# Kernel tuning notes

Measured on AMD Instinct MI355X. Metric: run time of the kernel, lower is better.

The kernel has to match this reference:

```python
import jax, jax.numpy as jnp
import numpy as np

K = 16
EPS = 1e-5
SLOPE = 0.2


def knn_idx(k, xyz_k, xyz_q):
    # xyz_k: (B,Nk,3), xyz_q: (B,Nq,3) -> (B,Nq,k) indices of k nearest in xyz_k
    d = (jnp.sum(xyz_q * xyz_q, -1, keepdims=True)
         - 2.0 * jnp.einsum('bqc,bkc->bqk', xyz_q, xyz_k)
         + jnp.sum(xyz_k * xyz_k, -1)[:, None, :])
    _, idx = jax.lax.top_k(-d, k)
    return idx


def graph_feature(coor_q, x_q, coor_k, x_k):
    # coor_*: (B,N*,3); x_q: (B,C,Nq); x_k: (B,C,Nk) -> (B,2C,Nq,K)
    idx = knn_idx(K, coor_k, coor_q)                      # (B,Nq,K)
    nbr = jax.vmap(lambda xk, i: xk[:, i])(x_k, idx)       # (B,C,Nq,K)
    xq = x_q[:, :, :, None]                                # (B,C,Nq,1)
    xq = jnp.broadcast_to(xq, nbr.shape)
    return jnp.concatenate([nbr - xq, xq], axis=1)


def group_norm(x, gamma, beta, groups=4):
    B, C, N, Kk = x.shape
    xg = x.reshape(B, groups, C // groups, N, Kk)
    mu = jnp.mean(xg, axis=(2, 3, 4), keepdims=True)
    var = jnp.var(xg, axis=(2, 3, 4), keepdims=True)
    xn = ((xg - mu) / jnp.sqrt(var + EPS)).reshape(B, C, N, Kk)
    return xn * gamma[None, :, None, None] + beta[None, :, None, None]


def cgl(f, W, gamma, beta):
    # 1x1 Conv2d (no bias) + GroupNorm(4) + LeakyReLU(0.2)
    y = jnp.einsum('oc,bcnk->bonk', W, f)
    return jax.nn.leaky_relu(group_norm(y, gamma, beta), SLOPE)


def fps(xyz, m):
    # furthest point sampling. xyz: (B,N,3) -> (B,m) int32
    B, N, _ = xyz.shape
    first = jnp.zeros((B,), jnp.int32)

    def body(carry, _):
        dist, last = carry
        lp = jnp.take_along_axis(xyz, last[:, None, None].astype(jnp.int32), axis=1)  # (B,1,3)
        d = jnp.sum((xyz - lp) ** 2, -1)
        dist = jnp.minimum(dist, d)
        nxt = jnp.argmax(dist, -1).astype(jnp.int32)
        return (dist, nxt), nxt

    init = (jnp.full((B, N), 1e10, jnp.float32), first)
    _, rest = jax.lax.scan(body, init, None, length=m - 1)  # (m-1,B)
    return jnp.concatenate([first[None, :], rest], axis=0).T  # (B,m)


def fps_downsample(coor, x, m):
    # coor: (B,N,3), x: (B,C,N) -> new_coor (B,3,m), new_x (B,C,m)
    idx = fps(coor, m)                                        # (B,m)
    new_coor = jnp.take_along_axis(coor, idx[:, :, None], axis=1).transpose(0, 2, 1)
    new_x = jnp.take_along_axis(x, idx[:, None, :], axis=2)
    return new_coor, new_x


def setup_inputs() -> dict:
    key = jax.random.key(0)
    ks = jax.random.split(key, 16)
    d = {
        'x': jax.random.normal(ks[0], (8, 4096, 3), jnp.float32),
        'num0': 2048, 'num1': 512, 'num2': 128,
        'w_in': jax.random.normal(ks[1], (8, 3), jnp.float32) * 0.3,
        'b_in': jnp.zeros((8,), jnp.float32),
    }
    layer_dims = {'1': (32, 16), '2': (64, 64), '4': (128, 128),
                  '5': (128, 256), '6': (256, 256), '7': (256, 512)}
    for i, (name, (o, c)) in enumerate(layer_dims.items()):
        d[f'w{name}'] = jax.random.normal(ks[2 + i], (o, c), jnp.float32) * (1.0 / np.sqrt(c))
        d[f'g{name}'] = jnp.ones((o,), jnp.float32)
        d[f'be{name}'] = jnp.zeros((o,), jnp.float32)
    return d


def reference(x, num0, num1, num2, w_in, b_in,
              w1, g1, be1, w2, g2, be2, w4, g4, be4,
              w5, g5, be5, w6, g6, be6, w7, g7, be7):
    xyz = x.transpose(0, 2, 1)                                # (B,3,N)
    coor = x                                                  # (B,N,3)
    f = jnp.einsum('oc,bcn->bon', w_in, xyz) + b_in[None, :, None]  # (B,8,N)

    f = cgl(graph_feature(coor, f, coor, f), w1, g1, be1)     # (B,32,N,K)
    f = jnp.max(f, axis=-1)                                   # (B,32,N)

    sp1, f_q = fps_downsample(coor, f, num0)                  # (B,3,n0),(B,32,n0)
    coor_d = sp1.transpose(0, 2, 1)                           # (B,n0,3)
    f = cgl(graph_feature(coor_d, f_q, coor, f), w2, g2, be2)
    stage1_feature = jnp.max(f, axis=-1)                      # (B,64,n0)
    coor = coor_d

    sp2, f_q = fps_downsample(coor, stage1_feature, num1)
    coor_d = sp2.transpose(0, 2, 1)
    f = cgl(graph_feature(coor_d, f_q, coor, stage1_feature), w4, g4, be4)
    f = jnp.max(f, axis=-1)                                   # (B,128,n1)
    f = cgl(graph_feature(coor_d, f, coor_d, f), w5, g5, be5)
    stage2_feature = jnp.max(f, axis=-1)                      # (B,128,n1)
    coor = coor_d

    sp3, f_q = fps_downsample(coor, stage2_feature, num2)
    coor_d = sp3.transpose(0, 2, 1)
    f = cgl(graph_feature(coor_d, f_q, coor, stage2_feature), w6, g6, be6)
    f = jnp.max(f, axis=-1)                                   # (B,256,n2)
    f = cgl(graph_feature(coor_d, f, coor_d, f), w7, g7, be7)
    stage3_feature = jnp.max(f, axis=-1)                      # (B,256,n2)

    out_coor = sp3.transpose(0, 2, 1)                         # (B,n2,3)
    out_f = stage3_feature.transpose(0, 2, 1)                 # (B,n2,256)
    return out_coor, out_f
```

## Files before the change

### kernel.cpp

```cpp
#include <hip/hip_runtime.h>
#include <hip/hip_bf16.h>
#include <math.h>

#define DEVI __device__ __forceinline__
typedef unsigned long long ull;
typedef float f32x2 __attribute__((ext_vector_type(2)));

DEVI f32x2 pk_sub(f32x2 a, f32x2 b){
  f32x2 r;
  asm("v_pk_add_f32 %0, %1, %2 neg_lo:[0,1] neg_hi:[0,1]" : "=v"(r) : "v"(a), "v"(b));
  return r;
}
DEVI f32x2 pk_mul(f32x2 a, f32x2 b){
  f32x2 r; asm("v_pk_mul_f32 %0, %1, %2" : "=v"(r) : "v"(a), "v"(b)); return r;
}
DEVI f32x2 pk_add(f32x2 a, f32x2 b){
  f32x2 r; asm("v_pk_add_f32 %0, %1, %2" : "=v"(r) : "v"(a), "v"(b)); return r;
}

template<int CTRL>
DEVI float dppmaxf(float x){
  float o = __int_as_float(__builtin_amdgcn_update_dpp(__float_as_int(x),__float_as_int(x),CTRL,0xF,0xF,false));
  return fmaxf(x,o);
}
template<int CTRL>
DEVI unsigned dppminu(unsigned x){
  unsigned o = (unsigned)__builtin_amdgcn_update_dpp((int)x,(int)x,CTRL,0xF,0xF,false);
  return (x < o) ? x : o;
}

template<int P>
DEVI void fps_stage(f32x2 (&px)[P/2], f32x2 (&py)[P/2], f32x2 (&pz)[P/2],
                    int m, float sx, float sy, float sz,
                    const float* cpx, const float* cpy, const float* cpz,
                    ull* mK,
                    int* ssel, float* snx, float* sny, float* snz, int tid)
{
  const int wv = tid>>6, lane = tid&63;
  float dist[P];
  #pragma unroll
  for (int p=0;p<P;p++) dist[p]=1e10f;
  if (tid==0){ ssel[0]=0; if (snx){ snx[0]=sx; sny[0]=sy; snz[0]=sz; } }
  #pragma unroll 1
  for (int it=1; it<m; it++){
    f32x2 vsx, vsy, vsz;
    vsx.x=sx; vsx.y=sx; vsy.x=sy; vsy.y=sy; vsz.x=sz; vsz.y=sz;
    float bv = -1.f;
    #pragma unroll
    for (int i=0;i<P/2;i++){
      f32x2 dx = pk_sub(px[i], vsx);
      f32x2 dy = pk_sub(py[i], vsy);
      f32x2 dz = pk_sub(pz[i], vsz);
      f32x2 s  = pk_add(pk_add(pk_mul(dx,dx), pk_mul(dy,dy)), pk_mul(dz,dz));
      float d0 = fminf(dist[2*i],   s.x);
      float d1 = fminf(dist[2*i+1], s.y);
      dist[2*i] = d0; dist[2*i+1] = d1;
      bv = fmaxf(bv, d0);
      bv = fmaxf(bv, d1);
    }
    int bidx = 0;
    #pragma unroll
    for (int p=P-1;p>=0;p--) if (dist[p]==bv) bidx = tid+(p<<8);
    float w = bv;
    w = dppmaxf<0x111>(w);
    w = dppmaxf<0x112>(w);
    w = dppmaxf<0x114>(w);
    w = dppmaxf<0x118>(w);
    w = dppmaxf<0x142>(w);
    w = dppmaxf<0x143>(w);
    float bvw = __uint_as_float((unsigned)__builtin_amdgcn_readlane(__float_as_int(w),63));
    unsigned cand = (bv == bvw) ? (unsigned)bidx : 0xFFFFFFFFu;
    cand = dppminu<0x111>(cand);
    cand = dppminu<0x112>(cand);
    cand = dppminu<0x114>(cand);
    cand = dppminu<0x118>(cand);
    cand = dppminu<0x142>(cand);
    cand = dppminu<0x143>(cand);
    const unsigned itu = (unsigned)it;
    ull* slot = mK + ((it&1)<<2);
    if (lane==63){
      unsigned lo = ((~cand & 0xFFFu)<<12) | itu;
      *(volatile ull*)(slot + wv) = ((ull)__float_as_uint(bvw)<<32) | (ull)lo;
    }
    ull k0,k1,k2,k3;
    for (;;){
      asm volatile("" ::: "memory");
      k0=slot[0]; k1=slot[1]; k2=slot[2]; k3=slot[3];
      unsigned chk = (((unsigned)k0 ^ itu) | ((unsigned)k1 ^ itu) |
                      ((unsigned)k2 ^ itu) | ((unsigned)k3 ^ itu)) & 0xFFFu;
      if (chk == 0u) break;
    }
    ull ka = (k1>k0)?k1:k0;
    ull kb = (k3>k2)?k3:k2;
    ull kw = (kb>ka)?kb:ka;
    int gi = (int)((~((unsigned)(kw & 0xffffffffull) >> 12)) & 0xFFFu);
    sx = cpx[gi]; sy = cpy[gi]; sz = cpz[gi];
    if (tid==0){
      ssel[it]=gi;
      if (snx){ snx[it]=sx; sny[it]=sy; snz[it]=sz; }
    }
  }
}

template<int CTRL>
DEVI void dppmin_fj(float& d, int& j){
  float od = __int_as_float(__builtin_amdgcn_update_dpp(__float_as_int(d),__float_as_int(d),CTRL,0xF,0xF,false));
  int   oj = __builtin_amdgcn_update_dpp(j,j,CTRL,0xF,0xF,false);
  bool tk = (od < d) || (od == d && oj < j);
  d = tk?od:d; j = tk?oj:j;
}

DEVI float dist_qk(const float* __restrict__ ckb, int j,
                   float qx, float qy, float qz, float sqq){
  float kx=ckb[3*j], ky=ckb[3*j+1], kz=ckb[3*j+2];
  float sk  = __fadd_rn(__fadd_rn(__fmul_rn(kx,kx),__fmul_rn(ky,ky)),
                        __fmul_rn(kz,kz));
  float dot = __fadd_rn(__fadd_rn(__fmul_rn(qx,kx),__fmul_rn(qy,ky)),
                        __fmul_rn(qz,kz));
  return __fadd_rn(__fsub_rn(sqq, __fmul_rn(2.0f,dot)), sk);
}

template<int NPL>
DEVI void knn_wave(const float* __restrict__ cq, int Nq,
                   const float* __restrict__ ck, int Nk,
                   int* __restrict__ idx_out, int b, int q, int lane)
{
  size_t r3 = ((size_t)b*Nq+q)*3;
  float qx=cq[r3], qy=cq[r3+1], qz=cq[r3+2];
  float sqq = __fadd_rn(__fadd_rn(__fmul_rn(qx,qx),__fmul_rn(qy,qy)),
                        __fmul_rn(qz,qz));
  constexpr int GS = (NPL < 8) ? NPL : 8;
  constexpr int NG = NPL / GS;
  float gv[NG]; int gj[NG];
  const float* ckb = ck + (size_t)b*Nk*3;
  ull exmask = 0;
  int dirtyg = -1;
  int myout = 0;
  #pragma unroll 1
  for (int r=0; r<16; r++){
    #pragma unroll
    for (int g=0; g<NG; g++){
      if (dirtyg < 0 || dirtyg == g){
        float nv=__int_as_float(0x7f800000); int nj=0x7fffffff;
        #pragma unroll
        for (int e=0; e<GS; e++){
          const int i = g*GS+e;
          int j = lane + (i<<6);
          float d = dist_qk(ckb, j, qx,qy,qz, sqq);
          bool rem = ((exmask >> i) & 1ull) == 0ull;
          if (rem && d < nv){ nv=d; nj=j; }
        }
        gv[g]=nv; gj[g]=nj;
      }
    }
    float lv = gv[0]; int lj = gj[0];
    #pragma unroll
    for (int g=1; g<NG; g++)
      if (gv[g]<lv || (gv[g]==lv && gj[g]<lj)){ lv=gv[g]; lj=gj[g]; }
    float rd = lv; int rj = lj;
    dppmin_fj<0x111>(rd,rj);
    dppmin_fj<0x112>(rd,rj);
    dppmin_fj<0x114>(rd,rj);
    dppmin_fj<0x118>(rd,rj);
    dppmin_fj<0x142>(rd,rj);
    dppmin_fj<0x143>(rd,rj);
    int wj = __builtin_amdgcn_readlane(rj,63);
    if (lane == r) myout = wj;
    if ((wj & 63) == lane) exmask |= (1ull << (wj>>6));
    dirtyg = (wj>>6)/GS;
  }
  if (lane<16) idx_out[((size_t)b*Nq+q)*16 + lane] = myout;
}

__global__ __launch_bounds__(256) void k_fps_knn1(
    const float* __restrict__ coords0,
    int* __restrict__ idx1, int* __restrict__ idx2, int* __restrict__ idx3,
    float* __restrict__ c1, float* __restrict__ c2, float* __restrict__ c3,
    float* __restrict__ out, int* __restrict__ knn1,
    const float* __restrict__ w_in, const float* __restrict__ b_in,
    const float* __restrict__ wl1, const float* __restrict__ wq1,
    float* __restrict__ yk, float* __restrict__ yq)
{
  __shared__ float s1x[4096], s1y[4096], s1z[4096];
  __shared__ float s2x[2048], s2y[2048], s2z[2048];
  __shared__ float s3x[512],  s3y[512],  s3z[512];
  __shared__ float s4x[128],  s4y[128],  s4z[128];
  __shared__ int   ssel[2048];
  __shared__ alignas(32) ull mK[8];
  if (blockIdx.x >= 8 + 8192){
    const int g = blockIdx.x - 8200;
    const int b = g >> 6, bx = g & 63;
    const int tid = threadIdx.x;
    float* sf = s1x;
    const float* xb = coords0 + (size_t)b*4096*3;
    const int row0 = bx*64;
    for (int i=tid; i<64*8; i+=256){
      int r = i >> 3, c = i & 7;
      int row = row0 + r;
      float cx=xb[row*3], cy=xb[row*3+1], cz=xb[row*3+2];
      float s = __fadd_rn(__fadd_rn(__fmul_rn(cx,w_in[c*3+0]),
                                    __fmul_rn(cy,w_in[c*3+1])),
                          __fmul_rn(cz,w_in[c*3+2]));
      sf[r*9 + c] = __fadd_rn(s, b_in[c]);
    }
    __syncthreads();
    const int o = tid & 31, rg = tid >> 5;
    float ak[8], aq[8];
    #pragma unroll
    for (int m=0;m<8;m++){ ak[m]=0.f; aq[m]=0.f; }
    const float* lp = wl1 + o;
    const float* qp = wq1 + o;
    const float* sfr = sf + rg*8*9;
    #pragma unroll
    for (int c=0;c<8;c++){
      float wl = lp[c*32];
      float wq = qp[c*32];
      #pragma unroll
      for (int m=0;m<8;m++){
        float xv = sfr[m*9 + c];
        ak[m] = fmaf(xv, wl, ak[m]);
        aq[m] = fmaf(xv, wq, aq[m]);
      }
    }
    size_t obase = ((size_t)b*4096 + row0 + rg*8)*32 + o;
    #pragma unroll
    for (int m=0;m<8;m++){
      yk[obase + (size_t)m*32] = ak[m];
      yq[obase + (size_t)m*32] = aq[m];
    }
    return;
  }
  if (blockIdx.x >= 8){
    int flat = blockIdx.x - 8;
    int b = flat >> 10, qb = flat & 1023;
    int q = qb*4 + (threadIdx.x>>6);
    knn_wave<64>(coords0, 4096, coords0, 4096, knn1, b, q, threadIdx.x&63);
    return;
  }
  const int b = blockIdx.x, tid = threadIdx.x;
  __builtin_amdgcn_s_setprio(3);
  const float* cb = coords0 + (size_t)b*4096*3;
  if (tid<8) mK[tid] = ~0ull;
  {
    f32x2 px[8], py[8], pz[8];
    #pragma unroll
    for (int i=0;i<8;i++){
      int j0 = tid + ((2*i)<<8), j1 = tid + ((2*i+1)<<8);
      float X0=cb[3*j0], Y0=cb[3*j0+1], Z0=cb[3*j0+2];
      float X1=cb[3*j1], Y1=cb[3*j1+1], Z1=cb[3*j1+2];
      px[i].x=X0; px[i].y=X1; py[i].x=Y0; py[i].y=Y1; pz[i].x=Z0; pz[i].y=Z1;
      s1x[j0]=X0; s1y[j0]=Y0; s1z[j0]=Z0;
      s1x[j1]=X1; s1y[j1]=Y1; s1z[j1]=Z1;
    }
    float sx=cb[0], sy=cb[1], sz=cb[2];
    __syncthreads();
    fps_stage<16>(px,py,pz, 2048, sx,sy,sz, s1x,s1y,s1z,
                  mK, ssel, s2x,s2y,s2z, tid);
  }
  __syncthreads();
  {
    float* c1b = c1 + (size_t)b*2048*3;
    for (int i=tid;i<2048;i+=256){
      idx1[b*2048+i]=ssel[i];
      c1b[3*i]=s2x[i]; c1b[3*i+1]=s2y[i]; c1b[3*i+2]=s2z[i];
    }
  }
  {
    f32x2 px[4], py[4], pz[4];
    #pragma unroll
    for (int i=0;i<4;i++){
      int j0 = tid + ((2*i)<<8), j1 = tid + ((2*i+1)<<8);
      px[i].x=s2x[j0]; px[i].y=s2x[j1];
      py[i].x=s2y[j0]; py[i].y=s2y[j1];
      pz[i].x=s2z[j0]; pz[i].y=s2z[j1];
    }
    float sx=s2x[0], sy=s2y[0], sz=s2z[0];
    __syncthreads();
    fps_stage<8>(px,py,pz, 512, sx,sy,sz, s2x,s2y,s2z,
                 mK, ssel, s3x,s3y,s3z, tid);
  }
  __syncthreads();
  {
    float* c2b = c2 + (size_t)b*512*3;
    for (int i=tid;i<512;i+=256){
      idx2[b*512+i]=ssel[i];
      c2b[3*i]=s3x[i]; c2b[3*i+1]=s3y[i]; c2b[3*i+2]=s3z[i];
    }
  }
  {
    f32x2 px[1], py[1], pz[1];
    {
      int j0 = tid, j1 = tid + 256;
      px[0].x=s3x[j0]; px[0].y=s3x[j1];
      py[0].x=s3y[j0]; py[0].y=s3y[j1];
      pz[0].x=s3z[j0]; pz[0].y=s3z[j1];
    }
    float sx=s3x[0], sy=s3y[0], sz=s3z[0];
    __syncthreads();
    fps_stage<2>(px,py,pz, 128, sx,sy,sz, s3x,s3y,s3z,
                 mK, ssel, s4x,s4y,s4z, tid);
  }
  __syncthreads();
  {
    float* c3b = c3 + (size_t)b*128*3;
    float* ob  = out + (size_t)b*128*3;
    for (int i=tid;i<128;i+=256){
      idx3[b*128+i]=ssel[i];
      float X=s4x[i],Y=s4y[i],Z=s4z[i];
      c3b[3*i]=X; c3b[3*i+1]=Y; c3b[3*i+2]=Z;
      ob[3*i]=X; ob[3*i+1]=Y; ob[3*i+2]=Z;
    }
  }
}

struct WtParams {
  const float* W[6];
  float* wl[6];
  float* wq[6];
  int O[6], C[6], OC[6];
};
__global__ void k_wt_all(WtParams p, float* __restrict__ stats){
  int s = blockIdx.y;
  int t = blockIdx.x*blockDim.x + threadIdx.x;
  if (s==0 && t<384) stats[t] = 0.f;
  int OC = p.OC[s];
  if (t >= OC) return;
  int C = p.C[s], O = p.O[s];
  int o = t / C, c = t - o*C;
  const float* W = p.W[s];
  float wlv = W[o*2*C + c];
  float wrv = W[o*2*C + C + c];
  p.wl[s][c*O+o] = wlv;
  p.wq[s][c*O+o] = wrv - wlv;
}

#define GEMM_M 8
template<int NPL>
__global__ __launch_bounds__(256,3) void k_knn_gemm(
    const float* __restrict__ cq, int Nq,
    const float* __restrict__ ck, int Nk, int* __restrict__ knnidx,
    const float* __restrict__ vmsrc,
    const float* __restrict__ stats, const float* __restrict__ gamma,
    const float* __restrict__ beta, float invcnt,
    int C, int O,
    const float* __restrict__ wlT, const float* __restrict__ wqT,
    float* __restrict__ yk, float* __restrict__ yq, int gknn)
{
  const int b = blockIdx.y;
  if ((int)blockIdx.x < gknn){
    int q = blockIdx.x*4 + (threadIdx.x>>6);
    if (q < Nq) knn_wave<NPL>(cq, Nq, ck, Nk, knnidx, b, q, threadIdx.x&63);
    return;
  }
  const int bx = blockIdx.x - gknn;
  extern __shared__ float sf[];
  const int o = threadIdx.x & (O-1);
  const int rg = threadIdx.x / O;
  const int R = blockDim.x / O;
  const int rowsPB = R*GEMM_M;
  const int row0 = bx * rowsPB;
  const int Cp = C+1;
  {
    const float* src = vmsrc + ((size_t)b*Nk + row0)*C;
    for (int i=threadIdx.x; i<rowsPB*C; i+=blockDim.x){
      int r = i / C, c = i - r*C;
      int g = (c*4)/C;
      float s1 = stats[b*8+g*2], s2 = stats[b*8+g*2+1];
      float mu = s1*invcnt;
      float var = fmaf(-mu,mu, s2*invcnt);
      float rs = 1.0f/sqrtf(var+1e-5f);
      float v = (src[i]-mu)*rs*gamma[c] + beta[c];
      sf[r*Cp + c] = (v>=0.f)? v : 0.2f*v;
    }
  }
  __syncthreads();
  float ak[GEMM_M], aq[GEMM_M];
  #pragma unroll
  for (int m=0;m<GEMM_M;m++){ ak[m]=0.f; aq[m]=0.f; }
  const float* lp = wlT + o;
  const float* qp = wqT + o;
  const float* sfr = sf + rg*GEMM_M*Cp;
  for (int c=0;c<C;c++){
    float wl = lp[(size_t)c*O];
    float wq = qp[(size_t)c*O];
    #pragma unroll
    for (int m=0;m<GEMM_M;m++){
      float xv = sfr[m*Cp + c];
      ak[m] = fmaf(xv, wl, ak[m]);
      aq[m] = fmaf(xv, wq, aq[m]);
    }
  }
  size_t obase = ((size_t)b*Nk + row0 + rg*GEMM_M)*O + o;
  #pragma unroll
  for (int m=0;m<GEMM_M;m++){
    yk[obase + (size_t)m*O] = ak[m];
    yq[obase + (size_t)m*O] = aq[m];
  }
}

__global__ void k_gather(const float* __restrict__ yk, const float* __restrict__ yq,
                         const int* __restrict__ knnidx, const int* __restrict__ qmap,
                         int Nq, int Nk, int O,
                         float* __restrict__ vmax, float* __restrict__ stats)
{
  const int b = blockIdx.y;
  const int o = threadIdx.x & (O-1);
  const int rg = threadIdx.x / O;
  const int R = blockDim.x / O;
  float ls=0.f, ls2=0.f;
  const float* ykb = yk + (size_t)b*Nk*O;
  const float* yqb = yq + (size_t)b*Nk*O;
  for (int nq = blockIdx.x*R + rg; nq < Nq; nq += gridDim.x*R){
    int qj = qmap ? qmap[b*Nq+nq] : nq;
    float vq = yqb[(size_t)qj*O + o];
    const int* ip = knnidx + ((size_t)b*Nq+nq)*16;
    float vmx = -3.4e38f;
    #pragma unroll
    for (int k=0;k<16;k++){
      int j = ip[k];
      float v = ykb[(size_t)j*O+o] + vq;
      vmx = fmaxf(vmx, v);
      ls += v; ls2 = fmaf(v,v,ls2);
    }
    vmax[((size_t)b*Nq+nq)*O+o] = vmx;
  }
  int span = O/4; if (span>64) span=64;
  for (int mm=1; mm<span; mm<<=1){
    ls  += __shfl_xor(ls, mm);
    ls2 += __shfl_xor(ls2, mm);
  }
  __shared__ float sred[8];
  if (threadIdx.x<8) sred[threadIdx.x]=0.f;
  __syncthreads();
  int lane = threadIdx.x & 63;
  if ((lane & (span-1))==0){
    int g = (o*4)/O;
    atomicAdd(&sred[g*2+0], ls);
    atomicAdd(&sred[g*2+1], ls2);
  }
  __syncthreads();
  if (threadIdx.x<8) atomicAdd(&stats[b*8+threadIdx.x], sred[threadIdx.x]);
}

__global__ void k_norm(const float* __restrict__ vmax, const float* __restrict__ stats,
                       const float* __restrict__ gamma,
                       const float* __restrict__ beta,
                       int Nq, int O, float invcnt, float* __restrict__ outf)
{
  const int b = blockIdx.y;
  const int n = Nq*O;
  for (int i = blockIdx.x*blockDim.x+threadIdx.x; i<n; i+=gridDim.x*blockDim.x){
    int o = i & (O-1);
    int g = (o*4)/O;
    float s1 = stats[b*8+g*2], s2 = stats[b*8+g*2+1];
    float mu = s1*invcnt;
    float var = fmaf(-mu,mu, s2*invcnt);
    float rs = 1.0f/sqrtf(var+1e-5f);
    float v = (vmax[(size_t)b*n + i]-mu)*rs*gamma[o] + beta[o];
    outf[(size_t)b*n + i] = (v>=0.f)? v : 0.2f*v;
  }
}

extern "C" void kernel_launch(void* const* d_in, const int* in_sizes, int n_in,
                              void* d_out, int out_size, void* d_ws, size_t ws_size,
                              hipStream_t stream)
{
  const int B = 8;
  const float* x    = (const float*)d_in[0];
  const float* w_in = (const float*)d_in[4];
  const float* b_in = (const float*)d_in[5];
  const float *Wm[6], *Gm[6], *Bm[6];
  for (int i=0;i<6;i++){
    Wm[i]=(const float*)d_in[6+3*i];
    Gm[i]=(const float*)d_in[6+3*i+1];
    Bm[i]=(const float*)d_in[6+3*i+2];
  }
  float* ws = (float*)d_ws;
  float* out = (float*)d_out;
  const size_t OFF_C1=4030464,  OFF_C2=4079616, OFF_C3=4091904,
               OFF_YK=4094976,  OFF_YQ=6192128, OFF_VM=8289280,
               OFF_WL=9337856,  OFF_WQ=9468928, OFF_ST=9600000,
               OFF_I1=9600384,  OFF_I2=9616768, OFF_I3=9620864, OFF_KNN=9621888,
               TOTAL=10146176;
  if (ws_size < TOTAL*sizeof(float)) return;
  float *c1=ws+OFF_C1, *c2=ws+OFF_C2, *c3=ws+OFF_C3,
        *yk=ws+OFF_YK, *yq=ws+OFF_YQ, *vm=ws+OFF_VM, *stats=ws+OFF_ST;
  int *i1=(int*)(ws+OFF_I1), *i2=(int*)(ws+OFF_I2), *i3=(int*)(ws+OFF_I3),
      *knn=(int*)(ws+OFF_KNN);

  const int OCs[6]  = {256, 2048, 8192, 16384, 32768, 65536};
  const int OCoff[6]= {0,   256,  2304, 10496, 26880, 59648};

  struct St { int C,O,Nk,Nq; const float* cq; const float* ck;
              const int* qmap; };
  const St st[6] = {
    {8,   32, 4096, 4096, x,  x,  nullptr},
    {32,  64, 4096, 2048, c1, x,  i1},
    {64, 128, 2048,  512, c2, c1, i2},
    {128,128,  512,  512, c2, c2, nullptr},
    {128,256,  512,  128, c3, c2, i3},
    {256,256,  128,  128, c3, c3, nullptr},
  };
  float invc[6];
  for (int s=0;s<6;s++)
    invc[s] = 1.0f / ((float)(st[s].O/4) * (float)st[s].Nq * 16.0f);

  WtParams wp;
  for (int s=0;s<6;s++){
    wp.W[s]=Wm[s];
    wp.wl[s]=ws+OFF_WL+OCoff[s];
    wp.wq[s]=ws+OFF_WQ+OCoff[s];
    wp.O[s]=st[s].O; wp.C[s]=st[s].C; wp.OC[s]=OCs[s];
  }
  k_wt_all<<<dim3(256,6), 256, 0, stream>>>(wp, stats);

  k_fps_knn1<<<8 + 8*1024 + 512, 256, 0, stream>>>(x, i1, i2, i3, c1, c2, c3,
                                                   out, knn,
                                                   w_in, b_in,
                                                   ws+OFF_WL, ws+OFF_WQ,
                                                   yk, yq);

  for (int s=0;s<6;s++){
    const St& S = st[s];
    if (s > 0){
      int rowsPB = 2048 / S.O;
      int ggemm = S.Nk / rowsPB;
      int gknn  = (S.Nq + 3)/4;
      dim3 gg(gknn + ggemm, B);
      size_t shb = (size_t)rowsPB * (S.C+1) * sizeof(float);
      const float* wl = ws+OFF_WL+OCoff[s];
      const float* wqp = ws+OFF_WQ+OCoff[s];
      const float* stp = stats + (s-1)*64;
      const float* gp  = Gm[s-1];
      const float* bp  = Bm[s-1];
      float ivc = invc[s-1];
      int npl = S.Nk >> 6;
      if      (npl == 64)
        k_knn_gemm<64><<<gg, 256, shb, stream>>>(S.cq,S.Nq,S.ck,S.Nk,knn,
          vm, stp, gp, bp, ivc, S.C, S.O, wl, wqp, yk, yq, gknn);
      else if (npl == 32)
        k_knn_gemm<32><<<gg, 256, shb, stream>>>(S.cq,S.Nq,S.ck,S.Nk,knn,
          vm, stp, gp, bp, ivc, S.C, S.O, wl, wqp, yk, yq, gknn);
      else if (npl ==  8)
        k_knn_gemm< 8><<<gg, 256, shb, stream>>>(S.cq,S.Nq,S.ck,S.Nk,knn,
          vm, stp, gp, bp, ivc, S.C, S.O, wl, wqp, yk, yq, gknn);
      else
        k_knn_gemm< 2><<<gg, 256, shb, stream>>>(S.cq,S.Nq,S.ck,S.Nk,knn,
          vm, stp, gp, bp, ivc, S.C, S.O, wl, wqp, yk, yq, gknn);
    }
    dim3 gs(64, B);
    k_gather<<<gs, 256, 0, stream>>>(yk, yq, knn, S.qmap, S.Nq, S.Nk, S.O,
                                     vm, stats + s*64);
  }
  {
    dim3 gn((128*256 + 255)/256, B);
    k_norm<<<gn, 256, 0, stream>>>(vm, stats + 5*64, Gm[5], Bm[5],
                                   128, 256, invc[5], out + 8*128*3);
  }
}
```

Before: 2.292 ms.

## Split FPS kernel and overlap later FPS stages with stage-0 gather and stage-1 kNN

The fused FPS kernel is split in two. The first kernel does the 4096→2048 sampling plus the stage-0 kNN and GEMM. A second kernel runs the 2048→512→128 sampling in 8 blocks, while other blocks in the same grid do the stage-0 gather/stats and the stage-1 kNN into a separate index buffer. This removes the serial tail in which only 8 blocks ran the deeper FPS stages while the GPU sat mostly idle. The cost is one more launch, and the second kNN buffer sits at workspace offset 0, which could alias other data.

```diff
diff --git a/kernel.cpp b/kernel.cpp
--- a/kernel.cpp
+++ b/kernel.cpp
@@ -172,19 +172,58 @@
   if (lane<16) idx_out[((size_t)b*Nq+q)*16 + lane] = myout;
 }
 
-__global__ __launch_bounds__(256) void k_fps_knn1(
+DEVI void gather_dev(const float* __restrict__ yk, const float* __restrict__ yq,
+                     const int* __restrict__ knnidx, const int* __restrict__ qmap,
+                     int Nq, int Nk, int O, int b, int bx, int gX,
+                     float* __restrict__ vmax, float* __restrict__ stats,
+                     float* sred, int tidx)
+{
+  const int o = tidx & (O-1);
+  const int rg = tidx / O;
+  const int R = 256 / O;
+  float ls=0.f, ls2=0.f;
+  const float* ykb = yk + (size_t)b*Nk*O;
+  const float* yqb = yq + (size_t)b*Nk*O;
+  for (int nq = bx*R + rg; nq < Nq; nq += gX*R){
+    int qj = qmap ? qmap[b*Nq+nq] : nq;
+    float vq = yqb[(size_t)qj*O + o];
+    const int* ip = knnidx + ((size_t)b*Nq+nq)*16;
+    float vmx = -3.4e38f;
+    #pragma unroll
+    for (int k=0;k<16;k++){
+      int j = ip[k];
+      float v = ykb[(size_t)j*O+o] + vq;
+      vmx = fmaxf(vmx, v);
+      ls += v; ls2 = fmaf(v,v,ls2);
+    }
+    vmax[((size_t)b*Nq+nq)*O+o] = vmx;
+  }
+  int span = O/4; if (span>64) span=64;
+  for (int mm=1; mm<span; mm<<=1){
+    ls  += __shfl_xor(ls, mm);
+    ls2 += __shfl_xor(ls2, mm);
+  }
+  if (tidx<8) sred[tidx]=0.f;
+  __syncthreads();
+  int lane = tidx & 63;
+  if ((lane & (span-1))==0){
+    int g = (o*4)/O;
+    atomicAdd(&sred[g*2+0], ls);
+    atomicAdd(&sred[g*2+1], ls2);
+  }
+  __syncthreads();
+  if (tidx<8) atomicAdd(&stats[b*8+tidx], sred[tidx]);
+}
+
+__global__ __launch_bounds__(256) void k_fps1(
     const float* __restrict__ coords0,
-    int* __restrict__ idx1, int* __restrict__ idx2, int* __restrict__ idx3,
-    float* __restrict__ c1, float* __restrict__ c2, float* __restrict__ c3,
-    float* __restrict__ out, int* __restrict__ knn1,
+    int* __restrict__ idx1, float* __restrict__ c1, int* __restrict__ knn1,
     const float* __restrict__ w_in, const float* __restrict__ b_in,
     const float* __restrict__ wl1, const float* __restrict__ wq1,
     float* __restrict__ yk, float* __restrict__ yq)
 {
   __shared__ float s1x[4096], s1y[4096], s1z[4096];
   __shared__ float s2x[2048], s2y[2048], s2z[2048];
-  __shared__ float s3x[512],  s3y[512],  s3z[512];
-  __shared__ float s4x[128],  s4y[128],  s4z[128];
   __shared__ int   ssel[2048];
   __shared__ alignas(32) ull mK[8];
   if (blockIdx.x >= 8 + 8192){
@@ -265,6 +304,47 @@
       c1b[3*i]=s2x[i]; c1b[3*i+1]=s2y[i]; c1b[3*i+2]=s2z[i];
     }
   }
+}
+
+__global__ __launch_bounds__(256) void k_fps23(
+    const float* __restrict__ coords0, const float* __restrict__ c1,
+    int* __restrict__ idx2, int* __restrict__ idx3,
+    float* __restrict__ c2, float* __restrict__ c3,
+    float* __restrict__ out,
+    const float* __restrict__ yk, const float* __restrict__ yq,
+    const int* __restrict__ knn1, float* __restrict__ vm,
+    float* __restrict__ stats0, int* __restrict__ knn2)
+{
+  __shared__ float s2x[2048], s2y[2048], s2z[2048];
+  __shared__ float s3x[512],  s3y[512],  s3z[512];
+  __shared__ float s4x[128],  s4y[128],  s4z[128];
+  __shared__ int   ssel[512];
+  __shared__ alignas(32) ull mK[8];
+  __shared__ float sred[8];
+  if (blockIdx.x >= 520){
+    int flat = blockIdx.x - 520;
+    int b = flat >> 9, qb = flat & 511;
+    int q = qb*4 + (threadIdx.x>>6);
+    knn_wave<64>(c1, 2048, coords0, 4096, knn2, b, q, threadIdx.x&63);
+    return;
+  }
+  if (blockIdx.x >= 8){
+    int g = blockIdx.x - 8;
+    int b = g >> 6, bx = g & 63;
+    gather_dev(yk, yq, knn1, nullptr, 4096, 4096, 32, b, bx, 64,
+               vm, stats0, sred, threadIdx.x);
+    return;
+  }
+  const int b = blockIdx.x, tid = threadIdx.x;
+  __builtin_amdgcn_s_setprio(3);
+  if (tid<8) mK[tid] = ~0ull;
+  {
+    const float* c1b = c1 + (size_t)b*2048*3;
+    for (int i=tid;i<2048;i+=256){
+      s2x[i]=c1b[3*i]; s2y[i]=c1b[3*i+1]; s2z[i]=c1b[3*i+2];
+    }
+  }
+  __syncthreads();
   {
     f32x2 px[4], py[4], pz[4];
     #pragma unroll
@@ -287,6 +367,7 @@
       c2b[3*i]=s3x[i]; c2b[3*i+1]=s3y[i]; c2b[3*i+2]=s3z[i];
     }
   }
+  __syncthreads();
   {
     f32x2 px[1], py[1], pz[1];
     {
@@ -403,43 +484,9 @@
                          int Nq, int Nk, int O,
                          float* __restrict__ vmax, float* __restrict__ stats)
 {
-  const int b = blockIdx.y;
-  const int o = threadIdx.x & (O-1);
-  const int rg = threadIdx.x / O;
-  const int R = blockDim.x / O;
-  float ls=0.f, ls2=0.f;
-  const float* ykb = yk + (size_t)b*Nk*O;
-  const float* yqb = yq + (size_t)b*Nk*O;
-  for (int nq = blockIdx.x*R + rg; nq < Nq; nq += gridDim.x*R){
-    int qj = qmap ? qmap[b*Nq+nq] : nq;
-    float vq = yqb[(size_t)qj*O + o];
-    const int* ip = knnidx + ((size_t)b*Nq+nq)*16;
-    float vmx = -3.4e38f;
-    #pragma unroll
-    for (int k=0;k<16;k++){
-      int j = ip[k];
-      float v = ykb[(size_t)j*O+o] + vq;
-      vmx = fmaxf(vmx, v);
-      ls += v; ls2 = fmaf(v,v,ls2);
-    }
-    vmax[((size_t)b*Nq+nq)*O+o] = vmx;
-  }
-  int span = O/4; if (span>64) span=64;
-  for (int mm=1; mm<span; mm<<=1){
-    ls  += __shfl_xor(ls, mm);
-    ls2 += __shfl_xor(ls2, mm);
-  }
   __shared__ float sred[8];
-  if (threadIdx.x<8) sred[threadIdx.x]=0.f;
-  __syncthreads();
-  int lane = threadIdx.x & 63;
-  if ((lane & (span-1))==0){
-    int g = (o*4)/O;
-    atomicAdd(&sred[g*2+0], ls);
-    atomicAdd(&sred[g*2+1], ls2);
-  }
-  __syncthreads();
-  if (threadIdx.x<8) atomicAdd(&stats[b*8+threadIdx.x], sred[threadIdx.x]);
+  gather_dev(yk, yq, knnidx, qmap, Nq, Nk, O,
+             blockIdx.y, blockIdx.x, gridDim.x, vmax, stats, sred, threadIdx.x);
 }
 
 __global__ void k_norm(const float* __restrict__ vmax, const float* __restrict__ stats,
@@ -477,7 +524,8 @@
   }
   float* ws = (float*)d_ws;
   float* out = (float*)d_out;
-  const size_t OFF_C1=4030464,  OFF_C2=4079616, OFF_C3=4091904,
+  const size_t OFF_KNN2=0,
+               OFF_C1=4030464,  OFF_C2=4079616, OFF_C3=4091904,
                OFF_YK=4094976,  OFF_YQ=6192128, OFF_VM=8289280,
                OFF_WL=9337856,  OFF_WQ=9468928, OFF_ST=9600000,
                OFF_I1=9600384,  OFF_I2=9616768, OFF_I3=9620864, OFF_KNN=9621888,
@@ -486,7 +534,7 @@
   float *c1=ws+OFF_C1, *c2=ws+OFF_C2, *c3=ws+OFF_C3,
         *yk=ws+OFF_YK, *yq=ws+OFF_YQ, *vm=ws+OFF_VM, *stats=ws+OFF_ST;
   int *i1=(int*)(ws+OFF_I1), *i2=(int*)(ws+OFF_I2), *i3=(int*)(ws+OFF_I3),
-      *knn=(int*)(ws+OFF_KNN);
+      *knn=(int*)(ws+OFF_KNN), *knn2=(int*)(ws+OFF_KNN2);
 
   const int OCs[6]  = {256, 2048, 8192, 16384, 32768, 65536};
   const int OCoff[6]= {0,   256,  2304, 10496, 26880, 59648};
@@ -514,42 +562,42 @@
   }
   k_wt_all<<<dim3(256,6), 256, 0, stream>>>(wp, stats);
 
-  k_fps_knn1<<<8 + 8*1024 + 512, 256, 0, stream>>>(x, i1, i2, i3, c1, c2, c3,
-                                                   out, knn,
-                                                   w_in, b_in,
-                                                   ws+OFF_WL, ws+OFF_WQ,
-                                                   yk, yq);
-
-  for (int s=0;s<6;s++){
+  k_fps1<<<8 + 8*1024 + 512, 256, 0, stream>>>(x, i1, c1, knn,
+                                               w_in, b_in,
+                                               ws+OFF_WL, ws+OFF_WQ,
+                                               yk, yq);
+  k_fps23<<<8 + 512 + 8*512, 256, 0, stream>>>(x, c1, i2, i3, c2, c3, out,
+                                               yk, yq, knn, vm, stats, knn2);
+
+  for (int s=1;s<6;s++){
     const St& S = st[s];
-    if (s > 0){
-      int rowsPB = 2048 / S.O;
-      int ggemm = S.Nk / rowsPB;
-      int gknn  = (S.Nq + 3)/4;
-      dim3 gg(gknn + ggemm, B);
-      size_t shb = (size_t)rowsPB * (S.C+1) * sizeof(float);
-      const float* wl = ws+OFF_WL+OCoff[s];
-      const float* wqp = ws+OFF_WQ+OCoff[s];
-      const float* stp = stats + (s-1)*64;
-      const float* gp  = Gm[s-1];
-      const float* bp  = Bm[s-1];
-      float ivc = invc[s-1];
-      int npl = S.Nk >> 6;
-      if      (npl == 64)
-        k_knn_gemm<64><<<gg, 256, shb, stream>>>(S.cq,S.Nq,S.ck,S.Nk,knn,
-          vm, stp, gp, bp, ivc, S.C, S.O, wl, wqp, yk, yq, gknn);
-      else if (npl == 32)
-        k_knn_gemm<32><<<gg, 256, shb, stream>>>(S.cq,S.Nq,S.ck,S.Nk,knn,
-          vm, stp, gp, bp, ivc, S.C, S.O, wl, wqp, yk, yq, gknn);
-      else if (npl ==  8)
-        k_knn_gemm< 8><<<gg, 256, shb, stream>>>(S.cq,S.Nq,S.ck,S.Nk,knn,
-          vm, stp, gp, bp, ivc, S.C, S.O, wl, wqp, yk, yq, gknn);
-      else
-        k_knn_gemm< 2><<<gg, 256, shb, stream>>>(S.cq,S.Nq,S.ck,S.Nk,knn,
-          vm, stp, gp, bp, ivc, S.C, S.O, wl, wqp, yk, yq, gknn);
-    }
+    int rowsPB = 2048 / S.O;
+    int ggemm = S.Nk / rowsPB;
+    int gknn  = (s == 1) ? 0 : (S.Nq + 3)/4;
+    dim3 gg(gknn + ggemm, B);
+    size_t shb = (size_t)rowsPB * (S.C+1) * sizeof(float);
+    const float* wl = ws+OFF_WL+OCoff[s];
+    const float* wqp = ws+OFF_WQ+OCoff[s];
+    const float* stp = stats + (s-1)*64;
+    const float* gp  = Gm[s-1];
+    const float* bp  = Bm[s-1];
+    float ivc = invc[s-1];
+    int npl = S.Nk >> 6;
+    if      (npl == 64)
+      k_knn_gemm<64><<<gg, 256, shb, stream>>>(S.cq,S.Nq,S.ck,S.Nk,knn,
+        vm, stp, gp, bp, ivc, S.C, S.O, wl, wqp, yk, yq, gknn);
+    else if (npl == 32)
+      k_knn_gemm<32><<<gg, 256, shb, stream>>>(S.cq,S.Nq,S.ck,S.Nk,knn,
+        vm, stp, gp, bp, ivc, S.C, S.O, wl, wqp, yk, yq, gknn);
+    else if (npl ==  8)
+      k_knn_gemm< 8><<<gg, 256, shb, stream>>>(S.cq,S.Nq,S.ck,S.Nk,knn,
+        vm, stp, gp, bp, ivc, S.C, S.O, wl, wqp, yk, yq, gknn);
+    else
+      k_knn_gemm< 2><<<gg, 256, shb, stream>>>(S.cq,S.Nq,S.ck,S.Nk,knn,
+        vm, stp, gp, bp, ivc, S.C, S.O, wl, wqp, yk, yq, gknn);
     dim3 gs(64, B);
-    k_gather<<<gs, 256, 0, stream>>>(yk, yq, knn, S.qmap, S.Nq, S.Nk, S.O,
+    const int* kidx = (s == 1) ? knn2 : knn;
+    k_gather<<<gs, 256, 0, stream>>>(yk, yq, kidx, S.qmap, S.Nq, S.Nk, S.O,
                                      vm, stats + s*64);
   }
   {
```

Result: faster. 2.132 ms (-7.0%).
